# Optimization experiments

Measured on AMD Instinct MI355X. Metric: run time of the kernel, lower is better.

## Reference

```python
import jax, jax.numpy as jnp
import numpy as np

N_NODES = 100000
N_EDGES = 1600000
IN_DIM = 128
HID_DIM = 64


def setup_inputs() -> dict:
    key = jax.random.key(0)
    ks = jax.random.split(key, 8)
    feat = jax.random.normal(ks[0], (N_NODES, IN_DIM), dtype=jnp.float32)
    # xavier-normal-like scaling for gcn weights
    w1 = jax.random.normal(ks[1], (IN_DIM, HID_DIM), dtype=jnp.float32) * np.sqrt(2.0 / (IN_DIM + HID_DIM))
    w2 = jax.random.normal(ks[2], (HID_DIM, HID_DIM), dtype=jnp.float32) * np.sqrt(2.0 / (HID_DIM + HID_DIM))
    conv_w = jax.random.normal(ks[3], (2, 1, 3), dtype=jnp.float32) * np.sqrt(2.0 / 3.0)
    conv_b = jax.random.uniform(ks[4], (2,), dtype=jnp.float32, minval=-1.0 / np.sqrt(3.0), maxval=1.0 / np.sqrt(3.0))
    ref_radius = jnp.zeros((1,), dtype=jnp.float32)
    src = jax.random.randint(ks[5], (N_EDGES,), 0, N_NODES, dtype=jnp.int32)
    dst = jax.random.randint(ks[6], (N_EDGES,), 0, N_NODES, dtype=jnp.int32)
    return {"feat": feat, "w1": w1, "w2": w2, "conv_w": conv_w, "conv_b": conv_b,
            "ref_radius": ref_radius, "src": src, "dst": dst}


def _dropout(h, key, p=0.5):
    keep = jax.random.bernoulli(key, 1.0 - p, h.shape)
    return jnp.where(keep, h / (1.0 - p), 0.0)


def _gcn(h, w, norm, src2, dst2, n, pre_matmul):
    # norm-scale -> (matmul) -> copy_src/sum scatter -> (matmul) -> norm-scale -> relu
    h = h * norm[:, None]
    if pre_matmul:  # in_feats > out_feats branch
        h = h @ w
        agg = jax.ops.segment_sum(h[src2], dst2, num_segments=n)
    else:
        agg = jax.ops.segment_sum(h[src2], dst2, num_segments=n)
        agg = agg @ w
    rst = agg * norm[:, None]
    return jax.nn.relu(rst)


def reference(feat, w1, w2, conv_w, conv_b, ref_radius, src, dst):
    n = feat.shape[0]
    # dgl.add_self_loop
    loops = jnp.arange(n, dtype=src.dtype)
    src2 = jnp.concatenate([src, loops])
    dst2 = jnp.concatenate([dst, loops])
    deg = jax.ops.segment_sum(jnp.ones_like(dst2, dtype=jnp.float32), dst2, num_segments=n)
    norm = jnp.clip(deg, 1.0, None) ** -0.5  # [n]

    dkey = jax.random.key(42)
    k1, k2 = jax.random.split(dkey)

    h = _gcn(feat, w1, norm, src2, dst2, n, pre_matmul=True)   # 128 > 64
    h = _dropout(h, k1)
    h = _gcn(h, w2, norm, src2, dst2, n, pre_matmul=False)     # 64 == 64
    h = _dropout(h, k2)

    # conv1d: [n, hid] -> [n, 1, hid] -> [n, 2, hid-2] -> [n, 2*(hid-2)]
    x = h[:, None, :]
    y = jax.lax.conv_general_dilated(x, conv_w, window_strides=(1,), padding='VALID',
                                     dimension_numbers=('NCH', 'OIH', 'NCH'))
    y = y + conv_b[None, :, None]
    h = y.reshape(n, -1)

    # hypersphere: distance of each node feature from the centroid vs ref radius
    o = jnp.mean(h, axis=0)
    radius = jnp.sqrt(jnp.sum((h - o + 1e-6) ** 2, axis=1))  # F.pairwise_distance eps=1e-6
    dis = jnp.clip(radius - ref_radius, 1e-4, 1.0 - 1e-4)
    return dis, ref_radius
```

## Files before the change

kernel.cpp:

```cpp
#include <hip/hip_runtime.h>
#include <stdint.h>

#define HID 64
#define INDIM 128
#define NBK 512
#define NBLK 512
#define EPBCAP 3200
#define BK3CAP 8192

typedef __attribute__((ext_vector_type(8))) short bf16x8;
typedef __attribute__((ext_vector_type(4))) float f32x4;
typedef __attribute__((ext_vector_type(2))) float f32x2;

__host__ __device__ __forceinline__ void tf2x32(uint32_t k0, uint32_t k1,
                                                uint32_t x0, uint32_t x1,
                                                uint32_t& o0, uint32_t& o1) {
  uint32_t ks2 = k0 ^ k1 ^ 0x1BD11BDAu;
#define ROTL(v, r) (((v) << (r)) | ((v) >> (32 - (r))))
#define RND(r) { x0 += x1; x1 = ROTL(x1, r); x1 ^= x0; }
  x0 += k0; x1 += k1;
  RND(13) RND(15) RND(26) RND(6)
  x0 += k1; x1 += ks2 + 1u;
  RND(17) RND(29) RND(16) RND(24)
  x0 += ks2; x1 += k0 + 2u;
  RND(13) RND(15) RND(26) RND(6)
  x0 += k0; x1 += k1 + 3u;
  RND(17) RND(29) RND(16) RND(24)
  x0 += k1; x1 += ks2 + 4u;
  RND(13) RND(15) RND(26) RND(6)
  x0 += ks2; x1 += k0 + 5u;
  o0 = x0; o1 = x1;
#undef RND
#undef ROTL
}

__device__ __forceinline__ float tf_uniform(uint32_t ka, uint32_t kb, uint32_t j) {
  uint32_t o0, o1;
  tf2x32(ka, kb, 0u, j, o0, o1);
  uint32_t bits = o0 ^ o1;
  uint32_t f = (bits >> 9) | 0x3f800000u;
  return __uint_as_float(f) - 1.0f;
}

__device__ __forceinline__ unsigned short f2bf(float f) {
  uint32_t x = __float_as_uint(f);
  uint32_t r = (x + 0x7fffu + ((x >> 16) & 1u)) >> 16;
  return (unsigned short)r;
}

__device__ __forceinline__ float bf2f_lo(uint32_t u) { return __uint_as_float(u << 16); }
__device__ __forceinline__ float bf2f_hi(uint32_t u) { return __uint_as_float(u & 0xffff0000u); }

__device__ __forceinline__ unsigned char f2fp8(float v) {
  return (unsigned char)(__builtin_amdgcn_cvt_pk_fp8_f32(v, 0.f, 0, false) & 0xff);
}

__global__ __launch_bounds__(256) void binsort_k(const int* __restrict__ src,
                                                 const int* __restrict__ dst,
                                                 uint32_t* __restrict__ sorted,
                                                 int* __restrict__ blockoff,
                                                 int E, int EPB, int NB) {
  __shared__ uint32_t lbuf[EPBCAP];
  __shared__ int ha[NBK], hb[NBK], cursor[NBK];
  int b = blockIdx.x, t = threadIdx.x;
  int e0 = b * EPB;
  int e1 = e0 + EPB; if (e1 > E) e1 = E;
  int m = e1 - e0;
  ha[t] = 0; ha[t + 256] = 0;
  __syncthreads();
  for (int i = t; i < m; i += 256) atomicAdd(&ha[dst[e0 + i] >> 8], 1);
  __syncthreads();
  int* cur = ha; int* nxt = hb;
  for (int off = 1; off < 512; off <<= 1) {
    int i0 = t, i1 = t + 256;
    int v0 = cur[i0] + ((i0 >= off) ? cur[i0 - off] : 0);
    int v1 = cur[i1] + ((i1 >= off) ? cur[i1 - off] : 0);
    __syncthreads();
    nxt[i0] = v0; nxt[i1] = v1;
    __syncthreads();
    int* tmp = cur; cur = nxt; nxt = tmp;
  }
  int* bo = blockoff + (size_t)b * (NB + 1);
  for (int i = t; i < NB; i += 256) {
    int ex = (i == 0) ? 0 : cur[i - 1];
    cursor[i] = ex;
    bo[i] = ex;
  }
  if (t == 0) bo[NB] = m;
  __syncthreads();
  for (int i = t; i < m; i += 256) {
    int d = dst[e0 + i], s = src[e0 + i];
    int pos = atomicAdd(&cursor[d >> 8], 1);
    lbuf[pos] = ((uint32_t)s << 8) | (uint32_t)(d & 255);
  }
  __syncthreads();
  for (int i = t; i < m; i += 256) sorted[e0 + i] = lbuf[i];
}

__global__ __launch_bounds__(NBLK) void boff_k(const int* __restrict__ blockoff,
                                               int* __restrict__ destoff,
                                               int* __restrict__ totals, int NB) {
  __shared__ int sa[NBK], sb[NBK];
  int k = blockIdx.x, t = threadIdx.x;
  const int stride = NB + 1;
  int len = blockoff[(size_t)t * stride + k + 1] - blockoff[(size_t)t * stride + k];
  sa[t] = len;
  __syncthreads();
  int* cur = sa; int* nxt = sb;
  for (int off = 1; off < NBLK; off <<= 1) {
    int v = cur[t] + ((t >= off) ? cur[t - off] : 0);
    __syncthreads();
    nxt[t] = v;
    __syncthreads();
    int* tmp = cur; cur = nxt; nxt = tmp;
  }
  destoff[(size_t)t * NB + k] = cur[t] - len;
  if (t == NBLK - 1) totals[k] = cur[t];
}

__global__ __launch_bounds__(512) void bscan_k(const int* __restrict__ totals,
                                               int* __restrict__ bucketstart,
                                               float* __restrict__ colsum,
                                               int NB, int E) {
  __shared__ int sa[NBK], sb[NBK];
  int t = threadIdx.x;
  int v = (t < NB) ? totals[t] : 0;
  sa[t] = v;
  __syncthreads();
  int* cur = sa; int* nxt = sb;
  for (int off = 1; off < 512; off <<= 1) {
    int x = cur[t] + ((t >= off) ? cur[t - off] : 0);
    __syncthreads();
    nxt[t] = x;
    __syncthreads();
    int* tmp = cur; cur = nxt; nxt = tmp;
  }
  if (t < NB) bucketstart[t] = cur[t] - v;
  if (t == 0) bucketstart[NB] = E;
  if (t < HID) colsum[t] = 0.f;
}

__global__ __launch_bounds__(256) void scatter2_k(const uint32_t* __restrict__ sorted,
                                                  const int* __restrict__ blockoff,
                                                  const int* __restrict__ destoff,
                                                  const int* __restrict__ bucketstart,
                                                  uint32_t* __restrict__ sorted2,
                                                  int EPB, int NB) {
  int b = blockIdx.x, t = threadIdx.x;
  const uint32_t* chunk = sorted + (size_t)b * EPB;
  const int* bo = blockoff + (size_t)b * (NB + 1);
  for (int k = t; k < NB; k += 256) {
    int ss = bo[k], se = bo[k + 1];
    int dd = bucketstart[k] + destoff[(size_t)b * NB + k];
    for (int i = ss; i < se; i++) sorted2[dd + (i - ss)] = chunk[i];
  }
}

__global__ __launch_bounds__(256) void csrbuild_k(const uint32_t* __restrict__ sorted2,
                                                  const int* __restrict__ bucketstart,
                                                  int* __restrict__ rowstart,
                                                  int* __restrict__ csr,
                                                  float* __restrict__ norm,
                                                  int NB, int n, int E) {
  __shared__ uint32_t ebuf[BK3CAP];
  __shared__ int sa[256], sb[256], cursor[256];
  int k = blockIdx.x, t = threadIdx.x;
  int s0 = bucketstart[k], s1 = bucketstart[k + 1];
  int M = s1 - s0;
  for (int i = t; i < M; i += 256) ebuf[i] = sorted2[s0 + i];
  cursor[t] = 0;
  __syncthreads();
  for (int i = t; i < M; i += 256) atomicAdd(&cursor[ebuf[i] & 255], 1);
  __syncthreads();
  int cnt = cursor[t];
  sa[t] = cnt;
  int* cur = sa; int* nxt = sb;
  __syncthreads();
  for (int off = 1; off < 256; off <<= 1) {
    int v = cur[t] + ((t >= off) ? cur[t - off] : 0);
    __syncthreads();
    nxt[t] = v;
    __syncthreads();
    int* tmp = cur; cur = nxt; nxt = tmp;
  }
  int localrow = cur[t] - cnt;
  int node = k * 256 + t;
  if (node < n) {
    rowstart[node] = s0 + localrow;
    norm[node] = rsqrtf((float)(cnt + 1));
  }
  if (k == NB - 1 && t == 255) rowstart[n] = E;
  cursor[t] = localrow;
  __syncthreads();
  for (int i = t; i < M; i += 256) {
    uint32_t pe = ebuf[i];
    int pos = atomicAdd(&cursor[pe & 255], 1);
    csr[s0 + pos] = (int)(pe >> 8);
  }
}

__global__ __launch_bounds__(256) void wcvt_k(const float* __restrict__ w1,
                                              const float* __restrict__ w2,
                                              unsigned short* __restrict__ w1t,
                                              unsigned short* __restrict__ w2t) {
  int i = blockIdx.x * 256 + threadIdx.x;
  if (i < INDIM * HID) {
    int c = i >> 7, k = i & 127;
    w1t[i] = f2bf(w1[k * HID + c]);
  } else {
    int j = i - INDIM * HID;
    if (j < HID * HID) {
      int c = j >> 6, k = j & 63;
      w2t[j] = f2bf(w2[k * HID + c]);
    }
  }
}

__global__ __launch_bounds__(256) void gemm1(const float* __restrict__ feat,
                                             const unsigned short* __restrict__ w1t,
                                             const float* __restrict__ norm,
                                             unsigned char* __restrict__ h0, int n) {
  int t = threadIdx.x;
  int wv = t >> 6, lane = t & 63;
  int strip = blockIdx.x * 4 + wv;
  if (strip * 16 >= n) return;
  int m = lane & 15, q = lane >> 4;
  bf16x8 Bf[4][4];
#pragma unroll
  for (int kc = 0; kc < 4; kc++)
#pragma unroll
    for (int ct = 0; ct < 4; ct++)
      Bf[kc][ct] = *(const bf16x8*)(w1t + (ct * 16 + m) * INDIM + kc * 32 + q * 8);
  const float* arow = feat + (size_t)(strip * 16 + m) * INDIM;
  bf16x8 Af[4];
#pragma unroll
  for (int kc = 0; kc < 4; kc++) {
    const float* pa = arow + kc * 32 + q * 8;
    bf16x8 a;
#pragma unroll
    for (int j = 0; j < 8; j++) a[j] = (short)f2bf(pa[j]);
    Af[kc] = a;
  }
  f32x4 acc[4] = {{0.f,0.f,0.f,0.f},{0.f,0.f,0.f,0.f},{0.f,0.f,0.f,0.f},{0.f,0.f,0.f,0.f}};
#pragma unroll
  for (int kc = 0; kc < 4; kc++)
#pragma unroll
    for (int ct = 0; ct < 4; ct++)
      acc[ct] = __builtin_amdgcn_mfma_f32_16x16x32_bf16(Af[kc], Bf[kc][ct], acc[ct], 0, 0, 0);
#pragma unroll
  for (int r = 0; r < 4; r++) {
    int row = strip * 16 + q * 4 + r;
    float nm = norm[row];
#pragma unroll
    for (int ct = 0; ct < 4; ct++)
      h0[(size_t)row * HID + ct * 16 + m] = f2fp8(acc[ct][r] * nm);
  }
}

template <int MODE>
__global__ __launch_bounds__(256) void gather_k(const uint32_t* __restrict__ h8,
                                                void* __restrict__ outp,
                                                const int* __restrict__ rowstart,
                                                const int* __restrict__ csr,
                                                const float* __restrict__ norm,
                                                int n, uint32_t ka, uint32_t kb) {
  int wid = (int)((blockIdx.x * 256u + threadIdx.x) >> 6);
  int d0 = wid * 4;
  if (d0 >= n) return;
  int lane = threadIdx.x & 63;
  int g = lane >> 4, c4 = lane & 15;
  int g4 = g << 2;

  int rr = d0 + (lane < 4 ? lane : 4);
  if (rr > n) rr = n;
  int rsl = rowstart[rr];
  int r0[5];
#pragma unroll
  for (int i = 0; i < 5; ++i) r0[i] = __shfl(rsl, i);
  int L[4];
#pragma unroll
  for (int i = 0; i < 4; ++i) L[i] = r0[i + 1] - r0[i];

  int selfrow = d0 + g; if (selfrow >= n) selfrow = d0;
  uint32_t uself = h8[(size_t)selfrow * 16 + c4];

  int idx[4];
#pragma unroll
  for (int i = 0; i < 4; ++i) {
    int la = L[i] < 32 ? L[i] : 32;
    idx[i] = (lane < la) ? csr[r0[i] + lane] : 0;
  }

  uint32_t u[4][8];
#pragma unroll
  for (int i = 0; i < 4; ++i) {
#pragma unroll
    for (int t = 0; t < 8; ++t) {
      int s = __builtin_amdgcn_ds_bpermute(16 * t + g4, idx[i]);
      u[i][t] = (4 * t + g < L[i]) ? h8[(size_t)(uint32_t)s * 16 + c4] : 0u;
    }
  }

  f32x2 al[4], ah[4];
#pragma unroll
  for (int i = 0; i < 4; ++i) { al[i] = (f32x2){0.f, 0.f}; ah[i] = (f32x2){0.f, 0.f}; }
#pragma unroll
  for (int i = 0; i < 4; ++i) {
#pragma unroll
    for (int t = 0; t < 8; ++t) {
      al[i] += __builtin_amdgcn_cvt_pk_f32_fp8((int)u[i][t], false);
      ah[i] += __builtin_amdgcn_cvt_pk_f32_fp8((int)u[i][t], true);
    }
  }

#pragma unroll
  for (int i = 0; i < 4; ++i) {
    if (L[i] > 32) {
      for (int e0 = 32; e0 < L[i]; e0 += 4) {
        int e = e0 + g;
        uint32_t uu = 0u;
        if (e < L[i]) {
          int s = csr[r0[i] + e];
          uu = h8[(size_t)(uint32_t)s * 16 + c4];
        }
        al[i] += __builtin_amdgcn_cvt_pk_f32_fp8((int)uu, false);
        ah[i] += __builtin_amdgcn_cvt_pk_f32_fp8((int)uu, true);
      }
    }
  }

  f32x2 sl, sh, rl2, rh2;
  sl = (g & 1) ? al[0] : al[1];
  sh = (g & 1) ? ah[0] : ah[1];
  rl2.x = __shfl_xor(sl.x, 16); rl2.y = __shfl_xor(sl.y, 16);
  rh2.x = __shfl_xor(sh.x, 16); rh2.y = __shfl_xor(sh.y, 16);
  f32x2 fABl = ((g & 1) ? al[1] : al[0]) + rl2;
  f32x2 fABh = ((g & 1) ? ah[1] : ah[0]) + rh2;
  sl = (g & 1) ? al[2] : al[3];
  sh = (g & 1) ? ah[2] : ah[3];
  rl2.x = __shfl_xor(sl.x, 16); rl2.y = __shfl_xor(sl.y, 16);
  rh2.x = __shfl_xor(sh.x, 16); rh2.y = __shfl_xor(sh.y, 16);
  f32x2 fCDl = ((g & 1) ? al[3] : al[2]) + rl2;
  f32x2 fCDh = ((g & 1) ? ah[3] : ah[2]) + rh2;
  sl = (g & 2) ? fABl : fCDl;
  sh = (g & 2) ? fABh : fCDh;
  rl2.x = __shfl_xor(sl.x, 32); rl2.y = __shfl_xor(sl.y, 32);
  rh2.x = __shfl_xor(sh.x, 32); rh2.y = __shfl_xor(sh.y, 32);
  f32x2 tl = ((g & 2) ? fCDl : fABl) + rl2;
  f32x2 th = ((g & 2) ? fCDh : fABh) + rh2;

  tl += __builtin_amdgcn_cvt_pk_f32_fp8((int)uself, false);
  th += __builtin_amdgcn_cvt_pk_f32_fp8((int)uself, true);

  int d = d0 + g;
  float a0 = tl.x, a1 = tl.y, a2 = th.x, a3 = th.y;
  if (MODE == 0) {
    uint32_t jb = (uint32_t)d0 * 64u + (uint32_t)lane;
    float u0 = tf_uniform(ka, kb, jb);
    float u1 = tf_uniform(ka, kb, jb + 64u);
    float u2 = tf_uniform(ka, kb, jb + 128u);
    float u3 = tf_uniform(ka, kb, jb + 192u);
    unsigned long long kp0 = __ballot(u0 < 0.5f);
    unsigned long long kp1 = __ballot(u1 < 0.5f);
    unsigned long long kp2 = __ballot(u2 < 0.5f);
    unsigned long long kp3 = __ballot(u3 < 0.5f);
    unsigned long long keep = (g & 2) ? ((g & 1) ? kp3 : kp2)
                                      : ((g & 1) ? kp1 : kp0);
    uint32_t kb4 = (uint32_t)(keep >> (4 * c4)) & 15u;
    float nm = norm[d < n ? d : d0];
    float v0 = fmaxf(a0 * nm, 0.f), v1 = fmaxf(a1 * nm, 0.f);
    float v2 = fmaxf(a2 * nm, 0.f), v3 = fmaxf(a3 * nm, 0.f);
    float s2 = 2.f * nm;
    v0 = (kb4 & 1u) ? v0 * s2 : 0.f;
    v1 = (kb4 & 2u) ? v1 * s2 : 0.f;
    v2 = (kb4 & 4u) ? v2 * s2 : 0.f;
    v3 = (kb4 & 8u) ? v3 * s2 : 0.f;
    if (d < n) {
      int o = __builtin_amdgcn_cvt_pk_fp8_f32(v0, v1, 0, false);
      o = __builtin_amdgcn_cvt_pk_fp8_f32(v2, v3, o, true);
      ((uint32_t*)outp)[(size_t)d * 16 + c4] = (uint32_t)o;
    }
  } else {
    if (d < n) {
      uint2 w;
      w.x = (uint32_t)f2bf(a0) | ((uint32_t)f2bf(a1) << 16);
      w.y = (uint32_t)f2bf(a2) | ((uint32_t)f2bf(a3) << 16);
      ((uint2*)outp)[(size_t)d * 16 + c4] = w;
    }
  }
}

__global__ __launch_bounds__(256) void gemm2(const unsigned short* __restrict__ aggbf,
                                             const unsigned short* __restrict__ w2t,
                                             const float* __restrict__ norm,
                                             unsigned short* __restrict__ h2, int n,
                                             uint32_t ka, uint32_t kb) {
  int t = threadIdx.x;
  int wv = t >> 6, lane = t & 63;
  int strip = blockIdx.x * 4 + wv;
  if (strip * 16 >= n) return;
  int m = lane & 15, q = lane >> 4;
  bf16x8 Bf[2][4];
#pragma unroll
  for (int kc = 0; kc < 2; kc++)
#pragma unroll
    for (int ct = 0; ct < 4; ct++)
      Bf[kc][ct] = *(const bf16x8*)(w2t + (ct * 16 + m) * HID + kc * 32 + q * 8);
  const unsigned short* arow = aggbf + (size_t)(strip * 16 + m) * HID;
  bf16x8 Af[2];
#pragma unroll
  for (int kc = 0; kc < 2; kc++)
    Af[kc] = *(const bf16x8*)(arow + kc * 32 + q * 8);
  f32x4 acc[4] = {{0.f,0.f,0.f,0.f},{0.f,0.f,0.f,0.f},{0.f,0.f,0.f,0.f},{0.f,0.f,0.f,0.f}};
#pragma unroll
  for (int kc = 0; kc < 2; kc++)
#pragma unroll
    for (int ct = 0; ct < 4; ct++)
      acc[ct] = __builtin_amdgcn_mfma_f32_16x16x32_bf16(Af[kc], Bf[kc][ct], acc[ct], 0, 0, 0);
#pragma unroll
  for (int r = 0; r < 4; r++) {
    int row = strip * 16 + q * 4 + r;
    float nm = norm[row];
#pragma unroll
    for (int ct = 0; ct < 4; ct++) {
      int col = ct * 16 + m;
      float v = fmaxf(acc[ct][r] * nm, 0.f);
      float u = tf_uniform(ka, kb, (uint32_t)row * 64u + (uint32_t)col);
      v = (u < 0.5f) ? v * 2.f : 0.f;
      h2[(size_t)row * HID + col] = f2bf(v);
    }
  }
}

__global__ __launch_bounds__(256) void colsum_k(const uint32_t* __restrict__ h2u,
                                                float* __restrict__ colsum, int n) {
  int t = threadIdx.x;
  int cp = t & 31;
  int rg = t >> 5;
  float sx = 0.f, sy = 0.f;
  for (int r = blockIdx.x * 8 + rg; r < n; r += gridDim.x * 8) {
    uint32_t u = h2u[(size_t)r * 32 + cp];
    sx += bf2f_lo(u); sy += bf2f_hi(u);
  }
  __shared__ float red[8][HID];
  red[rg][2 * cp] = sx; red[rg][2 * cp + 1] = sy;
  __syncthreads();
  if (t < HID) {
    float v = 0.f;
#pragma unroll
    for (int i = 0; i < 8; i++) v += red[i][t];
    atomicAdd(&colsum[t], v);
  }
}

__global__ __launch_bounds__(128) void final_k(const uint32_t* __restrict__ h2u,
                                               const float* __restrict__ colsum,
                                               const float* __restrict__ conv_w,
                                               const float* __restrict__ conv_b,
                                               const float* __restrict__ ref_radius,
                                               float* __restrict__ out, int n) {
  __shared__ float rows[128 * 67];
  __shared__ float omean[124];
  __shared__ float cm[HID];
  int t = threadIdx.x;
  int node0 = blockIdx.x * 128;
  if (t < HID) cm[t] = colsum[t] * (1.0f / (float)n);
  for (int idx = t; idx < 128 * 32; idx += 128) {
    int r = idx >> 5, cpi = idx & 31;
    int node = node0 + r;
    uint32_t u = (node < n) ? h2u[(size_t)node * 32 + cpi] : 0u;
    rows[r * 67 + 2 * cpi] = bf2f_lo(u);
    rows[r * 67 + 2 * cpi + 1] = bf2f_hi(u);
  }
  __syncthreads();
  if (t < 124) {
    int o = t / 62, i = t % 62;
    omean[t] = conv_b[o] + conv_w[o * 3] * cm[i] + conv_w[o * 3 + 1] * cm[i + 1] +
               conv_w[o * 3 + 2] * cm[i + 2];
  }
  __syncthreads();
  int node = node0 + t;
  if (node < n) {
    float r0[HID];
#pragma unroll
    for (int k = 0; k < HID; k++) r0[k] = rows[t * 67 + k];
    float w00 = conv_w[0], w01 = conv_w[1], w02 = conv_w[2];
    float w10 = conv_w[3], w11 = conv_w[4], w12 = conv_w[5];
    float b0 = conv_b[0], b1 = conv_b[1];
    float acc = 0.f;
#pragma unroll
    for (int i = 0; i < 62; i++) {
      float y0 = b0 + w00 * r0[i] + w01 * r0[i + 1] + w02 * r0[i + 2];
      float d0 = y0 - omean[i] + 1e-6f;
      acc += d0 * d0;
      float y1 = b1 + w10 * r0[i] + w11 * r0[i + 1] + w12 * r0[i + 2];
      float d1 = y1 - omean[62 + i] + 1e-6f;
      acc += d1 * d1;
    }
    float radius = sqrtf(acc);
    float dis = fminf(fmaxf(radius - ref_radius[0], 1e-4f), 1.f - 1e-4f);
    out[node] = dis;
  }
  if (blockIdx.x == 0 && t == 0) out[n] = ref_radius[0];
}

extern "C" void kernel_launch(void* const* d_in, const int* in_sizes, int n_in,
                              void* d_out, int out_size, void* d_ws, size_t ws_size,
                              hipStream_t stream) {
  const float* feat = (const float*)d_in[0];
  const float* w1 = (const float*)d_in[1];
  const float* w2 = (const float*)d_in[2];
  const float* conv_w = (const float*)d_in[3];
  const float* conv_b = (const float*)d_in[4];
  const float* ref_radius = (const float*)d_in[5];
  const int* src = (const int*)d_in[6];
  const int* dst = (const int*)d_in[7];
  int n = in_sizes[0] / INDIM;
  int E = in_sizes[6];
  float* out = (float*)d_out;

  int NB = (n + 255) >> 8;
  int EPB = (E + NBLK - 1) / NBLK;

  char* p = (char*)d_ws;
  auto carve = [&](size_t bytes) { void* r = (void*)p; p += (bytes + 255) & ~(size_t)255; return r; };
  float* norm = (float*)carve((size_t)n * 4);
  float* colsum = (float*)carve(HID * 4);
  int* rowstart = (int*)carve(((size_t)n + 1) * 4);
  int* bucketstart = (int*)carve(((size_t)NB + 1) * 4);
  int* totals = (int*)carve((size_t)NB * 4);
  int* blockoff = (int*)carve((size_t)NBLK * (NB + 1) * 4);
  int* destoff = (int*)carve((size_t)NBLK * NB * 4);
  uint32_t* sorted = (uint32_t*)carve((size_t)E * 4);
  uint32_t* sorted2 = (uint32_t*)carve((size_t)E * 4);
  int* csr = (int*)carve((size_t)E * 4);
  unsigned short* w1t = (unsigned short*)carve((size_t)INDIM * HID * 2);
  unsigned short* w2t = (unsigned short*)carve((size_t)HID * HID * 2);
  unsigned char* H0f8 = (unsigned char*)carve((size_t)n * HID);
  unsigned char* Tf8 = (unsigned char*)carve((size_t)n * HID);
  unsigned short* Abf = (unsigned short*)carve((size_t)n * HID * 2);
  unsigned short* H2bf = (unsigned short*)carve((size_t)n * HID * 2);

  uint32_t k1a, k1b, k2a, k2b;
  tf2x32(0u, 42u, 0u, 0u, k1a, k1b);
  tf2x32(0u, 42u, 0u, 1u, k2a, k2b);

  int gatherB = (n + 15) / 16;
  int stripB = ((n + 15) / 16 + 3) / 4;

  binsort_k<<<NBLK, 256, 0, stream>>>(src, dst, sorted, blockoff, E, EPB, NB);
  boff_k<<<NB, NBLK, 0, stream>>>(blockoff, destoff, totals, NB);
  bscan_k<<<1, 512, 0, stream>>>(totals, bucketstart, colsum, NB, E);
  scatter2_k<<<NBLK, 256, 0, stream>>>(sorted, blockoff, destoff, bucketstart, sorted2, EPB, NB);
  csrbuild_k<<<NB, 256, 0, stream>>>(sorted2, bucketstart, rowstart, csr, norm, NB, n, E);
  wcvt_k<<<(INDIM * HID + HID * HID + 255) / 256, 256, 0, stream>>>(w1, w2, w1t, w2t);
  gemm1<<<stripB, 256, 0, stream>>>(feat, w1t, norm, H0f8, n);
  gather_k<0><<<gatherB, 256, 0, stream>>>((const uint32_t*)H0f8, Tf8, rowstart, csr, norm, n, k1a, k1b);
  gather_k<1><<<gatherB, 256, 0, stream>>>((const uint32_t*)Tf8, Abf, rowstart, csr, norm, n, 0u, 0u);
  gemm2<<<stripB, 256, 0, stream>>>(Abf, w2t, norm, H2bf, n, k2a, k2b);
  colsum_k<<<256, 256, 0, stream>>>((const uint32_t*)H2bf, colsum, n);
  final_k<<<(n + 127) / 128, 128, 0, stream>>>((const uint32_t*)H2bf, colsum, conv_w, conv_b, ref_radius, out, n);
}
```

Measured before the change: 266.6 us.

## Fuse bucket scatter into CSR build and transpose block offset layout

Removes the scatter2 kernel and the sorted2 buffer. Each CSR-build block now gathers its bucket's edges directly from every binsort chunk into shared memory, using transposed (bucket-major) blockoff and destoff arrays so the offset reads are coalesced. Binsort caches dst in shared memory to avoid reading it twice, and CSR blocks are remapped so contiguous buckets land on the same XCD. This saves one kernel launch and a full round trip of the edge array through global memory. In exchange, each CSR block walks 512 short, scattered segment copies, with each thread copying its segments serially.

```diff
diff --git a/kernel.cpp b/kernel.cpp
--- a/kernel.cpp
+++ b/kernel.cpp
@@ -58,9 +58,10 @@
 __global__ __launch_bounds__(256) void binsort_k(const int* __restrict__ src,
                                                  const int* __restrict__ dst,
                                                  uint32_t* __restrict__ sorted,
-                                                 int* __restrict__ blockoff,
+                                                 int* __restrict__ blockoff2,
                                                  int E, int EPB, int NB) {
   __shared__ uint32_t lbuf[EPBCAP];
+  __shared__ int dbuf[EPBCAP];
   __shared__ int ha[NBK], hb[NBK], cursor[NBK];
   int b = blockIdx.x, t = threadIdx.x;
   int e0 = b * EPB;
@@ -68,7 +69,11 @@
   int m = e1 - e0;
   ha[t] = 0; ha[t + 256] = 0;
   __syncthreads();
-  for (int i = t; i < m; i += 256) atomicAdd(&ha[dst[e0 + i] >> 8], 1);
+  for (int i = t; i < m; i += 256) {
+    int d = dst[e0 + i];
+    dbuf[i] = d;
+    atomicAdd(&ha[d >> 8], 1);
+  }
   __syncthreads();
   int* cur = ha; int* nxt = hb;
   for (int off = 1; off < 512; off <<= 1) {
@@ -80,16 +85,15 @@
     __syncthreads();
     int* tmp = cur; cur = nxt; nxt = tmp;
   }
-  int* bo = blockoff + (size_t)b * (NB + 1);
   for (int i = t; i < NB; i += 256) {
     int ex = (i == 0) ? 0 : cur[i - 1];
     cursor[i] = ex;
-    bo[i] = ex;
-  }
-  if (t == 0) bo[NB] = m;
+    blockoff2[(size_t)i * NBLK + b] = ex;
+  }
+  if (t == 0) blockoff2[(size_t)NB * NBLK + b] = m;
   __syncthreads();
   for (int i = t; i < m; i += 256) {
-    int d = dst[e0 + i], s = src[e0 + i];
+    int d = dbuf[i], s = src[e0 + i];
     int pos = atomicAdd(&cursor[d >> 8], 1);
     lbuf[pos] = ((uint32_t)s << 8) | (uint32_t)(d & 255);
   }
@@ -97,13 +101,12 @@
   for (int i = t; i < m; i += 256) sorted[e0 + i] = lbuf[i];
 }
 
-__global__ __launch_bounds__(NBLK) void boff_k(const int* __restrict__ blockoff,
+__global__ __launch_bounds__(NBLK) void boff_k(const int* __restrict__ blockoff2,
                                                int* __restrict__ destoff,
                                                int* __restrict__ totals, int NB) {
   __shared__ int sa[NBK], sb[NBK];
   int k = blockIdx.x, t = threadIdx.x;
-  const int stride = NB + 1;
-  int len = blockoff[(size_t)t * stride + k + 1] - blockoff[(size_t)t * stride + k];
+  int len = blockoff2[(size_t)(k + 1) * NBLK + t] - blockoff2[(size_t)k * NBLK + t];
   sa[t] = len;
   __syncthreads();
   int* cur = sa; int* nxt = sb;
@@ -114,7 +117,7 @@
     __syncthreads();
     int* tmp = cur; cur = nxt; nxt = tmp;
   }
-  destoff[(size_t)t * NB + k] = cur[t] - len;
+  destoff[(size_t)k * NBLK + t] = cur[t] - len;
   if (t == NBLK - 1) totals[k] = cur[t];
 }
 
@@ -140,34 +143,29 @@
   if (t < HID) colsum[t] = 0.f;
 }
 
-__global__ __launch_bounds__(256) void scatter2_k(const uint32_t* __restrict__ sorted,
-                                                  const int* __restrict__ blockoff,
+__global__ __launch_bounds__(256) void csrbuild_k(const uint32_t* __restrict__ sorted,
+                                                  const int* __restrict__ blockoff2,
                                                   const int* __restrict__ destoff,
-                                                  const int* __restrict__ bucketstart,
-                                                  uint32_t* __restrict__ sorted2,
-                                                  int EPB, int NB) {
-  int b = blockIdx.x, t = threadIdx.x;
-  const uint32_t* chunk = sorted + (size_t)b * EPB;
-  const int* bo = blockoff + (size_t)b * (NB + 1);
-  for (int k = t; k < NB; k += 256) {
-    int ss = bo[k], se = bo[k + 1];
-    int dd = bucketstart[k] + destoff[(size_t)b * NB + k];
-    for (int i = ss; i < se; i++) sorted2[dd + (i - ss)] = chunk[i];
-  }
-}
-
-__global__ __launch_bounds__(256) void csrbuild_k(const uint32_t* __restrict__ sorted2,
                                                   const int* __restrict__ bucketstart,
                                                   int* __restrict__ rowstart,
                                                   int* __restrict__ csr,
                                                   float* __restrict__ norm,
-                                                  int NB, int n, int E) {
+                                                  int NB, int n, int E, int EPB) {
   __shared__ uint32_t ebuf[BK3CAP];
   __shared__ int sa[256], sb[256], cursor[256];
-  int k = blockIdx.x, t = threadIdx.x;
+  int bid = blockIdx.x, t = threadIdx.x;
+  int xcd = bid & 7, sub = bid >> 3;
+  int q = NB >> 3, r = NB & 7;
+  int k = (xcd < r ? xcd * (q + 1) : r * (q + 1) + (xcd - r) * q) + sub;
   int s0 = bucketstart[k], s1 = bucketstart[k + 1];
   int M = s1 - s0;
-  for (int i = t; i < M; i += 256) ebuf[i] = sorted2[s0 + i];
+  for (int b = t; b < NBLK; b += 256) {
+    int sb_ = blockoff2[(size_t)k * NBLK + b];
+    int se_ = blockoff2[(size_t)(k + 1) * NBLK + b];
+    int dd = destoff[(size_t)k * NBLK + b];
+    const uint32_t* sp = sorted + (size_t)b * EPB;
+    for (int i = sb_; i < se_; i++) ebuf[dd + (i - sb_)] = sp[i];
+  }
   cursor[t] = 0;
   __syncthreads();
   for (int i = t; i < M; i += 256) atomicAdd(&cursor[ebuf[i] & 255], 1);
@@ -529,10 +527,9 @@
   int* rowstart = (int*)carve(((size_t)n + 1) * 4);
   int* bucketstart = (int*)carve(((size_t)NB + 1) * 4);
   int* totals = (int*)carve((size_t)NB * 4);
-  int* blockoff = (int*)carve((size_t)NBLK * (NB + 1) * 4);
-  int* destoff = (int*)carve((size_t)NBLK * NB * 4);
+  int* blockoff2 = (int*)carve((size_t)(NB + 1) * NBLK * 4);
+  int* destoff = (int*)carve((size_t)NB * NBLK * 4);
   uint32_t* sorted = (uint32_t*)carve((size_t)E * 4);
-  uint32_t* sorted2 = (uint32_t*)carve((size_t)E * 4);
   int* csr = (int*)carve((size_t)E * 4);
   unsigned short* w1t = (unsigned short*)carve((size_t)INDIM * HID * 2);
   unsigned short* w2t = (unsigned short*)carve((size_t)HID * HID * 2);
@@ -548,11 +545,10 @@
   int gatherB = (n + 15) / 16;
   int stripB = ((n + 15) / 16 + 3) / 4;
 
-  binsort_k<<<NBLK, 256, 0, stream>>>(src, dst, sorted, blockoff, E, EPB, NB);
-  boff_k<<<NB, NBLK, 0, stream>>>(blockoff, destoff, totals, NB);
+  binsort_k<<<NBLK, 256, 0, stream>>>(src, dst, sorted, blockoff2, E, EPB, NB);
+  boff_k<<<NB, NBLK, 0, stream>>>(blockoff2, destoff, totals, NB);
   bscan_k<<<1, 512, 0, stream>>>(totals, bucketstart, colsum, NB, E);
-  scatter2_k<<<NBLK, 256, 0, stream>>>(sorted, blockoff, destoff, bucketstart, sorted2, EPB, NB);
-  csrbuild_k<<<NB, 256, 0, stream>>>(sorted2, bucketstart, rowstart, csr, norm, NB, n, E);
+  csrbuild_k<<<NB, 256, 0, stream>>>(sorted, blockoff2, destoff, bucketstart, rowstart, csr, norm, NB, n, E, EPB);
   wcvt_k<<<(INDIM * HID + HID * HID + 255) / 256, 256, 0, stream>>>(w1, w2, w1t, w2t);
   gemm1<<<stripB, 256, 0, stream>>>(feat, w1t, norm, H0f8, n);
   gather_k<0><<<gatherB, 256, 0, stream>>>((const uint32_t*)H0f8, Tf8, rowstart, csr, norm, n, k1a, k1b);
```

Result: faster. 256.8 us (-3.7%).
